# Performance work log

Hardware: AMD Instinct MI355X
Metric: run time of the kernel (lower is better)

Reference implementation:

```python
import jax, jax.numpy as jnp
import numpy as np

B, S, D, H = 8, 512, 1024, 8
DPH = D // H            # 128, dim per head
MAX_REL = 32
NGRAM = 2               # 2-gram RNN on heads 4..7
NG_START, NG_COUNT = 4, 4
SCALE = float(DPH) ** 0.5


def setup_inputs() -> dict:
    key = jax.random.key(0)
    ks = jax.random.split(key, 12)
    w = lambda k, shp: jax.random.normal(k, shp, jnp.float32) * 0.02
    return {
        "x": jax.random.normal(ks[0], (B, S, D), jnp.float32),
        "mask": jax.random.randint(ks[1], (B, 1, S), 0, 2).astype(bool),
        "Wq": w(ks[2], (D, D)), "bq": jnp.zeros((D,), jnp.float32),
        "Wk": w(ks[3], (D, D)), "bk": jnp.zeros((D,), jnp.float32),
        "Wv": w(ks[4], (D, D)), "bv": jnp.zeros((D,), jnp.float32),
        "Wo": w(ks[5], (D, D)), "bo": jnp.zeros((D,), jnp.float32),
        "rel_emb": w(ks[6], (2 * MAX_REL + 1, DPH)),
        "Wih_f": w(ks[7], (DPH, DPH)), "Whh_f": w(ks[8], (DPH, DPH)),
        "bih_f": jnp.zeros((DPH,), jnp.float32), "bhh_f": jnp.zeros((DPH,), jnp.float32),
        "Wih_b": w(ks[9], (DPH, DPH)), "Whh_b": w(ks[10], (DPH, DPH)),
        "bih_b": jnp.zeros((DPH,), jnp.float32), "bhh_b": jnp.zeros((DPH,), jnp.float32),
    }


def reference(x, mask, Wq, bq, Wk, bk, Wv, bv, Wo, bo, rel_emb,
              Wih_f, Whh_f, bih_f, bhh_f, Wih_b, Whh_b, bih_b, bhh_b):
    shape_h = lambda t: t.reshape(B, S, H, DPH).transpose(0, 2, 1, 3)  # [B,H,S,d]
    q = shape_h(x @ Wq.T + bq)
    k = shape_h(x @ Wk.T + bk)
    v = shape_h(x @ Wv.T + bv)

    # --- ngram path: zero masked positions in q/k/v (all heads) ---
    m = mask[:, :, :, None]  # [B,1,S,1] broadcast over heads and d
    q = jnp.where(m, 0.0, q)
    k = jnp.where(m, 0.0, k)
    v = jnp.where(m, 0.0, v)

    # per-head 2-gram bidirectional RNN on heads NG_START..NG_START+NG_COUNT-1
    qh = q[:, NG_START:NG_START + NG_COUNT].reshape(-1, S, DPH)
    kh = k[:, NG_START:NG_START + NG_COUNT].reshape(-1, S, DPH)
    vh = v[:, NG_START:NG_START + NG_COUNT].reshape(-1, S, DPH)
    feats = jnp.concatenate([qh, kh, vh], axis=0)          # [3*B*NG_COUNT, S, d]
    shifted = jnp.pad(feats, ((0, 0), (1, 0), (0, 0)))[:, :-1]  # shift-by-1 (prev token)
    seq = jnp.stack([shifted, feats], axis=0).reshape(NGRAM, -1, DPH)  # [T, N*S, d]
    h0 = jnp.zeros((seq.shape[1], DPH), jnp.float32)
    fstep = lambda h, xt: (jnp.tanh(xt @ Wih_f.T + bih_f + h @ Whh_f.T + bhh_f), None)
    bstep = lambda h, xt: (jnp.tanh(xt @ Wih_b.T + bih_b + h @ Whh_b.T + bhh_b), None)
    hf, _ = jax.lax.scan(fstep, h0, seq)            # fwd final hidden
    hb, _ = jax.lax.scan(bstep, h0, seq[::-1])      # bwd final hidden
    yy = (hf + hb).reshape(3, B, NG_COUNT, S, DPH)  # sum of direction finals
    q = q.at[:, NG_START:NG_START + NG_COUNT].set(yy[0])
    k = k.at[:, NG_START:NG_START + NG_COUNT].set(yy[1])
    v = v.at[:, NG_START:NG_START + NG_COUNT].set(yy[2])

    # --- relative-position attention ---
    qs = q / SCALE
    r = jnp.arange(S)
    rel_idx = jnp.clip(r[None, :] - r[:, None], -MAX_REL, MAX_REL) + MAX_REL  # [S,S]
    rel_k = rel_emb[rel_idx]  # [S,S,d]; same table used for keys and values
    scores = jnp.einsum('bhqd,bhkd->bhqk', qs, k) + jnp.einsum('bhqd,qkd->bhqk', qs, rel_k)
    scores = jnp.where(mask[:, None], -1e18, scores)  # [B,1,1,S] broadcast
    attn = jax.nn.softmax(scores, axis=-1)
    ctx = jnp.einsum('bhqk,bhkd->bhqd', attn, v) + jnp.einsum('bhqk,qkd->bhqd', attn, rel_k)
    out = ctx.transpose(0, 2, 1, 3).reshape(B, S, D) @ Wo.T + bo
    return out, attn
```

## Files before the change

### kernel.cpp

```cpp
#include <hip/hip_runtime.h>


typedef __bf16 bf16x8 __attribute__((ext_vector_type(8)));
typedef float f32x4 __attribute__((ext_vector_type(4)));

#define MFMA16(a, b, c) __builtin_amdgcn_mfma_f32_16x16x32_bf16(a, b, c, 0, 0, 0)

__device__ __forceinline__ unsigned short f2bf(float f) {
  unsigned u = __float_as_uint(f);
  u += 0x7FFFu + ((u >> 16) & 1u);
  return (unsigned short)(u >> 16);
}
__device__ __forceinline__ uint2 pack4(float4 f) {
  uint2 r;
  r.x = (unsigned)f2bf(f.x) | ((unsigned)f2bf(f.y) << 16);
  r.y = (unsigned)f2bf(f.z) | ((unsigned)f2bf(f.w) << 16);
  return r;
}
__device__ __forceinline__ void gld16(const unsigned short* g, unsigned short* l) {
  __builtin_amdgcn_global_load_lds(
      (const __attribute__((address_space(1))) unsigned int*)g,
      (__attribute__((address_space(3))) unsigned int*)l, 16, 0, 0);
}

__global__ __launch_bounds__(256) void prep_bf16(
    const float* __restrict__ x,
    const float* __restrict__ Wq, const float* __restrict__ Wk,
    const float* __restrict__ Wv,
    const float* __restrict__ Wihf, const float* __restrict__ Whhf,
    const float* __restrict__ Wihb, const float* __restrict__ Whhb,
    unsigned short* __restrict__ xb, unsigned short* __restrict__ Wqkvb,
    unsigned short* __restrict__ Wrnnb) {
  int i = blockIdx.x * 256 + threadIdx.x;
  const float* src;
  unsigned short* dst;
  int off;
  if (i < 1048576) {
    src = x; dst = xb; off = i;
  } else if (i < 1310720) {
    src = Wq; dst = Wqkvb; off = i - 1048576;
  } else if (i < 1572864) {
    src = Wk; dst = Wqkvb + 1048576; off = i - 1310720;
  } else if (i < 1835008) {
    src = Wv; dst = Wqkvb + 2097152; off = i - 1572864;
  } else if (i < 1839104) {
    src = Wihf; dst = Wrnnb; off = i - 1835008;
  } else if (i < 1843200) {
    src = Whhf; dst = Wrnnb + 16384; off = i - 1839104;
  } else if (i < 1847296) {
    src = Wihb; dst = Wrnnb + 32768; off = i - 1843200;
  } else {
    src = Whhb; dst = Wrnnb + 49152; off = i - 1847296;
  }
  float4 f = *((const float4*)src + off);
  *(uint2*)(dst + (size_t)off * 4) = pack4(f);
}

__global__ __launch_bounds__(256) void qkv_proj(
    const unsigned short* __restrict__ xb, const unsigned short* __restrict__ Wqkvb,
    const float* __restrict__ bq, const float* __restrict__ bk,
    const float* __restrict__ bv, const int* __restrict__ mask,
    unsigned short* __restrict__ qb, unsigned short* __restrict__ kb,
    unsigned short* __restrict__ vb, unsigned short* __restrict__ vT) {
  __shared__ __align__(16) unsigned short As[128 * 64];
  __shared__ __align__(16) unsigned short Bs[128 * 64];
  const int bm = blockIdx.x & 31;
  const int bn = blockIdx.x >> 5;
  const int t = bn >> 3;
  const int nloc0 = (bn & 7) * 128;
  const unsigned short* W = Wqkvb + (size_t)t * 1048576;
  const float* bias = (t == 0) ? bq : (t == 1) ? bk : bv;
  const int tid = threadIdx.x;
  const int lane = tid & 63, w = tid >> 6;
  const int wm = (w >> 1) * 64, wn = (w & 1) * 64;
  const int lanelo = lane & 15, quad = lane >> 4;
  const int row0 = bm * 128;
  const int rloc = lane >> 3, pch = lane & 7;
  const int lch = (pch - rloc) & 7;

  f32x4 acc[4][4];
  const f32x4 zf = {0.f, 0.f, 0.f, 0.f};
#pragma unroll
  for (int i = 0; i < 4; ++i)
#pragma unroll
    for (int j = 0; j < 4; ++j) acc[i][j] = zf;

  for (int kt = 0; kt < 16; ++kt) {
#pragma unroll
    for (int q = 0; q < 4; ++q) {
      int seg = w * 4 + q;
      int grow = seg * 8 + rloc;
      gld16(xb + (size_t)(row0 + grow) * 1024 + kt * 64 + lch * 8, &As[seg * 512]);
      gld16(W + (size_t)(nloc0 + grow) * 1024 + kt * 64 + lch * 8, &Bs[seg * 512]);
    }
    __syncthreads();
#pragma unroll
    for (int ks = 0; ks < 2; ++ks) {
      const int pA = (ks * 4 + quad + lanelo) & 7;
      bf16x8 a[4], bb[4];
#pragma unroll
      for (int i = 0; i < 4; ++i)
        a[i] = *(const bf16x8*)(&As[(wm + i * 16 + lanelo) * 64 + pA * 8]);
#pragma unroll
      for (int j = 0; j < 4; ++j)
        bb[j] = *(const bf16x8*)(&Bs[(wn + j * 16 + lanelo) * 64 + pA * 8]);
#pragma unroll
      for (int i = 0; i < 4; ++i)
#pragma unroll
        for (int j = 0; j < 4; ++j) acc[i][j] = MFMA16(a[i], bb[j], acc[i][j]);
    }
    __syncthreads();
  }
#pragma unroll
  for (int i = 0; i < 4; ++i) {
#pragma unroll
    for (int j = 0; j < 4; ++j) {
      int jj = nloc0 + wn + j * 16 + lanelo;
      int hh = jj >> 7, dc = jj & 127;
      float bvv = bias[jj];
      int m0 = row0 + wm + i * 16 + quad * 4;
      int b0 = m0 >> 9, sS = m0 & 511;
      unsigned short ov[4];
#pragma unroll
      for (int r = 0; r < 4; ++r) {
        int s = sS + r;
        float val = acc[i][j][r] + bvv;
        if (mask[b0 * 512 + s]) val = 0.f;
        unsigned short o = f2bf(val);
        ov[r] = o;
        size_t off = ((size_t)(b0 * 8 + hh) * 512 + s) * 128 + dc;
        if (t == 0) qb[off] = o;
        else if (t == 1) kb[off] = o;
        else vb[off] = o;
      }
      if (t == 2) {
        uint2 pk;
        pk.x = (unsigned)ov[0] | ((unsigned)ov[1] << 16);
        pk.y = (unsigned)ov[2] | ((unsigned)ov[3] << 16);
        *(uint2*)(&vT[((size_t)(b0 * 8 + hh) * 128 + dc) * 512 + sS]) = pk;
      }
    }
  }
}

__global__ __launch_bounds__(256) void prep_rel(
    const float* __restrict__ rel, unsigned short* __restrict__ relb,
    unsigned short* __restrict__ relT) {
  int i = blockIdx.x * 256 + threadIdx.x;
  if (i < 65 * 128) relb[i] = f2bf(rel[i]);
  if (i < 128 * 96) {
    int d = i / 96, r = i - d * 96;
    relT[i] = (r < 65) ? f2bf(rel[r * 128 + d]) : (unsigned short)0;
  }
}

__global__ __launch_bounds__(256) void rnn_fused(
    const unsigned short* __restrict__ qb, const unsigned short* __restrict__ kb,
    const unsigned short* __restrict__ vb,
    const unsigned short* __restrict__ Wrnnb,
    const float* __restrict__ bihf, const float* __restrict__ bhhf,
    const float* __restrict__ bihb, const float* __restrict__ bhhb,
    unsigned short* __restrict__ rnn_out) {
  __shared__ __align__(16) unsigned short X[65 * 136];
  __shared__ __align__(16) unsigned short Wi[128 * 136];
  __shared__ __align__(16) unsigned short Wh[128 * 136];
  __shared__ __align__(16) unsigned short H1[64 * 136];
  __shared__ float cbf[128], cbb[128];

  const unsigned short* Wihfb = Wrnnb;
  const unsigned short* Whhfb = Wrnnb + 16384;
  const unsigned short* Wihbb = Wrnnb + 32768;
  const unsigned short* Whhbb = Wrnnb + 49152;

  const int gid = blockIdx.x;
  const int tile = gid & 7;
  const int g = gid >> 3;
  const int t = g >> 5;
  const int rem = g & 31;
  const int b = rem >> 2, h = (rem & 3) + 4;
  const int s0 = tile * 64;
  const unsigned short* src = (t == 0) ? qb : (t == 1) ? kb : vb;
  const size_t rowbase = (size_t)(b * 8 + h) * 512;
  const int tid = threadIdx.x;

  for (int c = tid; c < 65 * 16; c += 256) {
    int r = c >> 4, cc = c & 15;
    uint4 v4;
    if (r == 0 && s0 == 0) v4 = make_uint4(0, 0, 0, 0);
    else v4 = *(const uint4*)(src + (rowbase + (s0 - 1 + r)) * 128 + cc * 8);
    *(uint4*)(&X[r * 136 + cc * 8]) = v4;
  }
#pragma unroll
  for (int p = 0; p < 8; ++p) {
    int c = p * 256 + tid;
    int r = c >> 4, cc = c & 15;
    *(uint4*)(&Wi[r * 136 + cc * 8]) = *(const uint4*)(Wihfb + c * 8);
    *(uint4*)(&Wh[r * 136 + cc * 8]) = *(const uint4*)(Whhfb + c * 8);
  }
  if (tid < 128) {
    cbf[tid] = bihf[tid] + bhhf[tid];
    cbb[tid] = bihb[tid] + bhhb[tid];
  }
  __syncthreads();

  const int lane = tid & 63, w = tid >> 6;
  const int lanelo = lane & 15, quad = lane >> 4;
  const int marow = w * 16 + lanelo;
  const f32x4 zf = {0.f, 0.f, 0.f, 0.f};

  f32x4 g1[8];
#pragma unroll
  for (int j = 0; j < 8; ++j) g1[j] = zf;
#pragma unroll
  for (int ks = 0; ks < 4; ++ks) {
    bf16x8 a = *(const bf16x8*)(&X[marow * 136 + ks * 32 + quad * 8]);
#pragma unroll
    for (int j = 0; j < 8; ++j) {
      bf16x8 bb = *(const bf16x8*)(&Wi[(j * 16 + lanelo) * 136 + ks * 32 + quad * 8]);
      g1[j] = MFMA16(a, bb, g1[j]);
    }
  }
#pragma unroll
  for (int j = 0; j < 8; ++j) {
    int col = j * 16 + lanelo;
    float cb = cbf[col];
#pragma unroll
    for (int i = 0; i < 4; ++i) {
      int row = w * 16 + quad * 4 + i;
      H1[row * 136 + col] = f2bf(tanhf(g1[j][i] + cb));
    }
  }
  __syncthreads();
  f32x4 a2[8];
#pragma unroll
  for (int j = 0; j < 8; ++j) a2[j] = zf;
#pragma unroll
  for (int ks = 0; ks < 4; ++ks) {
    bf16x8 a = *(const bf16x8*)(&X[(marow + 1) * 136 + ks * 32 + quad * 8]);
#pragma unroll
    for (int j = 0; j < 8; ++j) {
      bf16x8 bb = *(const bf16x8*)(&Wi[(j * 16 + lanelo) * 136 + ks * 32 + quad * 8]);
      a2[j] = MFMA16(a, bb, a2[j]);
    }
  }
#pragma unroll
  for (int ks = 0; ks < 4; ++ks) {
    bf16x8 a = *(const bf16x8*)(&H1[marow * 136 + ks * 32 + quad * 8]);
#pragma unroll
    for (int j = 0; j < 8; ++j) {
      bf16x8 bb = *(const bf16x8*)(&Wh[(j * 16 + lanelo) * 136 + ks * 32 + quad * 8]);
      a2[j] = MFMA16(a, bb, a2[j]);
    }
  }
  float outF[8][4];
#pragma unroll
  for (int j = 0; j < 8; ++j) {
    int col = j * 16 + lanelo;
    float cb = cbf[col];
#pragma unroll
    for (int i = 0; i < 4; ++i) outF[j][i] = tanhf(a2[j][i] + cb);
  }
  __syncthreads();
#pragma unroll
  for (int p = 0; p < 8; ++p) {
    int c = p * 256 + tid;
    int r = c >> 4, cc = c & 15;
    *(uint4*)(&Wi[r * 136 + cc * 8]) = *(const uint4*)(Wihbb + c * 8);
    *(uint4*)(&Wh[r * 136 + cc * 8]) = *(const uint4*)(Whhbb + c * 8);
  }
  __syncthreads();
#pragma unroll
  for (int j = 0; j < 8; ++j) g1[j] = zf;
#pragma unroll
  for (int ks = 0; ks < 4; ++ks) {
    bf16x8 a = *(const bf16x8*)(&X[(marow + 1) * 136 + ks * 32 + quad * 8]);
#pragma unroll
    for (int j = 0; j < 8; ++j) {
      bf16x8 bb = *(const bf16x8*)(&Wi[(j * 16 + lanelo) * 136 + ks * 32 + quad * 8]);
      g1[j] = MFMA16(a, bb, g1[j]);
    }
  }
#pragma unroll
  for (int j = 0; j < 8; ++j) {
    int col = j * 16 + lanelo;
    float cb = cbb[col];
#pragma unroll
    for (int i = 0; i < 4; ++i) {
      int row = w * 16 + quad * 4 + i;
      H1[row * 136 + col] = f2bf(tanhf(g1[j][i] + cb));
    }
  }
  __syncthreads();
#pragma unroll
  for (int j = 0; j < 8; ++j) a2[j] = zf;
#pragma unroll
  for (int ks = 0; ks < 4; ++ks) {
    bf16x8 a = *(const bf16x8*)(&X[marow * 136 + ks * 32 + quad * 8]);
#pragma unroll
    for (int j = 0; j < 8; ++j) {
      bf16x8 bb = *(const bf16x8*)(&Wi[(j * 16 + lanelo) * 136 + ks * 32 + quad * 8]);
      a2[j] = MFMA16(a, bb, a2[j]);
    }
  }
#pragma unroll
  for (int ks = 0; ks < 4; ++ks) {
    bf16x8 a = *(const bf16x8*)(&H1[marow * 136 + ks * 32 + quad * 8]);
#pragma unroll
    for (int j = 0; j < 8; ++j) {
      bf16x8 bb = *(const bf16x8*)(&Wh[(j * 16 + lanelo) * 136 + ks * 32 + quad * 8]);
      a2[j] = MFMA16(a, bb, a2[j]);
    }
  }
#pragma unroll
  for (int j = 0; j < 8; ++j) {
    int col = j * 16 + lanelo;
    float cb = cbb[col];
#pragma unroll
    for (int i = 0; i < 4; ++i) {
      int row = w * 16 + quad * 4 + i;
      float val = outF[j][i] + tanhf(a2[j][i] + cb);
      rnn_out[((size_t)g * 512 + s0 + row) * 128 + col] = f2bf(val);
    }
  }
}

__global__ __launch_bounds__(256) void rnn_copyback(
    const unsigned short* __restrict__ rnn_out,
    unsigned short* __restrict__ qb, unsigned short* __restrict__ kb,
    unsigned short* __restrict__ vT) {
  int idx = blockIdx.x * 256 + threadIdx.x;
  int g = idx >> 16;
  int r2 = idx & 65535;
  int s = r2 >> 7, col = r2 & 127;
  int t = g >> 5, rem = g & 31, b = rem >> 2, h = (rem & 3) + 4;
  unsigned short val = rnn_out[idx];
  size_t off = ((size_t)(b * 8 + h) * 512 + s) * 128 + col;
  if (t == 0) qb[off] = val;
  else if (t == 1) kb[off] = val;
  else vT[((size_t)(b * 8 + h) * 128 + col) * 512 + s] = val;
}

__global__ __launch_bounds__(256) void scores_av_fused(
    const unsigned short* __restrict__ qbuf, const unsigned short* __restrict__ kbuf,
    const unsigned short* __restrict__ relb, const unsigned short* __restrict__ vT,
    const unsigned short* __restrict__ relT, const float* __restrict__ relf,
    const int* __restrict__ mask, float* __restrict__ attn_out,
    unsigned short* __restrict__ ctx) {
  __shared__ __align__(16) char smem[40960];
  unsigned short* As = (unsigned short*)smem;
  float* Ps = (float*)(smem + 8704);
  float* cmaskS = (float*)(smem + 19456);
  unsigned short* attnb = (unsigned short*)smem;
  unsigned short* abufT = (unsigned short*)(smem + 32768);
  float* redb = (float*)(smem + 36864);

  const int idx = blockIdx.x;
  const int qt = idx >> 6, bh = idx & 63, b = bh >> 3;
  const int q0 = qt * 32;
  const size_t qrow0 = (size_t)bh * 512 + q0;
  const int tid = threadIdx.x;
  const int lane = tid & 63, w = tid >> 6;
  const int lanelo = lane & 15, quad = lane >> 4;
  const f32x4 zf = {0.f, 0.f, 0.f, 0.f};

  for (int c = tid; c < 512; c += 256) {
    int r = c >> 4, cc = c & 15;
    *(uint4*)(&As[r * 136 + cc * 8]) = *(const uint4*)(qbuf + (qrow0 + r) * 128 + cc * 8);
  }
  for (int i = tid; i < 512; i += 256) cmaskS[i] = mask[b * 512 + i] ? -1e9f : 0.f;
  if (tid < 256) *(uint4*)(&abufT[tid * 8]) = make_uint4(0, 0, 0, 0);
  __syncthreads();

  if (w < 2) {
    f32x4 pacc[5];
#pragma unroll
    for (int j = 0; j < 5; ++j) pacc[j] = zf;
#pragma unroll
    for (int ks = 0; ks < 4; ++ks) {
      bf16x8 qf_ = *(const bf16x8*)(&As[(w * 16 + lanelo) * 136 + ks * 32 + quad * 8]);
#pragma unroll
      for (int j = 0; j < 5; ++j) {
        int r = j * 16 + lanelo;
        uint4 tmp = make_uint4(0, 0, 0, 0);
        if (r < 65) tmp = *(const uint4*)(relb + r * 128 + ks * 32 + quad * 8);
        bf16x8 rf_ = *(bf16x8*)&tmp;
        pacc[j] = MFMA16(rf_, qf_, pacc[j]);
      }
    }
#pragma unroll
    for (int j = 0; j < 5; ++j)
      *(f32x4*)(&Ps[(w * 16 + lanelo) * 84 + j * 16 + quad * 4]) = pacc[j];
  }
  __syncthreads();

  f32x4 acc[8][2];
#pragma unroll
  for (int kf = 0; kf < 8; ++kf)
#pragma unroll
    for (int nf = 0; nf < 2; ++nf) acc[kf][nf] = zf;
  const unsigned short* kbp = kbuf + (size_t)bh * 65536;
#pragma unroll
  for (int ks = 0; ks < 4; ++ks) {
    bf16x8 qfr[2];
#pragma unroll
    for (int nf = 0; nf < 2; ++nf)
      qfr[nf] = *(const bf16x8*)(&As[(nf * 16 + lanelo) * 136 + ks * 32 + quad * 8]);
    bf16x8 kfr[8];
#pragma unroll
    for (int kf = 0; kf < 8; ++kf)
      kfr[kf] = *(const bf16x8*)(kbp + (size_t)((w * 8 + kf) * 16 + lanelo) * 128 +
                                 ks * 32 + quad * 8);
#pragma unroll
    for (int kf = 0; kf < 8; ++kf)
#pragma unroll
      for (int nf = 0; nf < 2; ++nf) acc[kf][nf] = MFMA16(kfr[kf], qfr[nf], acc[kf][nf]);
  }

  const float rscale = 0.08838834764831845f;
  float pmax[2] = {-3e38f, -3e38f};
#pragma unroll
  for (int qf = 0; qf < 2; ++qf) {
    const int q = qf * 16 + lanelo;
    const int qg = q0 + q;
    const float* PsR = &Ps[q * 84];
    const float p0 = PsR[0], p64 = PsR[64];
    const int qgmin = q0 + qf * 16;
#pragma unroll
    for (int kf = 0; kf < 8; ++kf) {
      const int kmin = w * 128 + kf * 16;
      const int kbase = kmin + quad * 4;
      if (kmin + 15 - qgmin <= -32) {
#pragma unroll
        for (int i = 0; i < 4; ++i) {
          float val = (acc[kf][qf][i] + p0) * rscale + cmaskS[kbase + i];
          acc[kf][qf][i] = val;
          pmax[qf] = fmaxf(pmax[qf], val);
        }
      } else if (kmin - (qgmin + 15) >= 32) {
#pragma unroll
        for (int i = 0; i < 4; ++i) {
          float val = (acc[kf][qf][i] + p64) * rscale + cmaskS[kbase + i];
          acc[kf][qf][i] = val;
          pmax[qf] = fmaxf(pmax[qf], val);
        }
      } else {
#pragma unroll
        for (int i = 0; i < 4; ++i) {
          int k = kbase + i;
          int d = k - qg;
          int r = min(max(d, -32), 32) + 32;
          float val = (acc[kf][qf][i] + PsR[r]) * rscale + cmaskS[k];
          acc[kf][qf][i] = val;
          pmax[qf] = fmaxf(pmax[qf], val);
        }
      }
    }
  }
  float* red_max = redb;
  float* red_sum = redb + 256;
  float* red_s0 = redb + 512;
  float* red_s64 = redb + 768;
#pragma unroll
  for (int qf = 0; qf < 2; ++qf) {
    pmax[qf] = fmaxf(pmax[qf], __shfl_xor(pmax[qf], 16, 64));
    pmax[qf] = fmaxf(pmax[qf], __shfl_xor(pmax[qf], 32, 64));
  }
  if (quad == 0) {
#pragma unroll
    for (int qf = 0; qf < 2; ++qf) red_max[w * 64 + qf * 16 + lanelo] = pmax[qf];
  }
  __syncthreads();
  float mf_[2], psum[2];
#pragma unroll
  for (int qf = 0; qf < 2; ++qf) {
    int q = qf * 16 + lanelo;
    mf_[qf] = fmaxf(fmaxf(red_max[q], red_max[64 + q]),
                    fmaxf(red_max[128 + q], red_max[192 + q]));
    psum[qf] = 0.f;
  }
#pragma unroll
  for (int qf = 0; qf < 2; ++qf)
#pragma unroll
    for (int kf = 0; kf < 8; ++kf)
#pragma unroll
      for (int i = 0; i < 4; ++i) {
        float e = __expf(acc[kf][qf][i] - mf_[qf]);
        acc[kf][qf][i] = e;
        psum[qf] += e;
      }
#pragma unroll
  for (int qf = 0; qf < 2; ++qf) {
    psum[qf] += __shfl_xor(psum[qf], 16, 64);
    psum[qf] += __shfl_xor(psum[qf], 32, 64);
  }
  if (quad == 0) {
#pragma unroll
    for (int qf = 0; qf < 2; ++qf) red_sum[w * 64 + qf * 16 + lanelo] = psum[qf];
  }
  __syncthreads();
  float rs[2];
#pragma unroll
  for (int qf = 0; qf < 2; ++qf) {
    int q = qf * 16 + lanelo;
    float s = red_sum[q] + red_sum[64 + q] + red_sum[128 + q] + red_sum[192 + q];
    rs[qf] = (s > 0.f) ? 1.f / s : 0.f;
  }

  float s0p[2] = {0.f, 0.f}, s64p[2] = {0.f, 0.f};
#pragma unroll
  for (int qf = 0; qf < 2; ++qf) {
    const int q = qf * 16 + lanelo;
    const int qg = q0 + q;
    const int qgmin = q0 + qf * 16;
#pragma unroll
    for (int kf = 0; kf < 8; ++kf) {
      const int kmin = w * 128 + kf * 16;
      const int kbase = kmin + quad * 4;
      float4 at;
      float* ap = (float*)&at;
#pragma unroll
      for (int i = 0; i < 4; ++i) ap[i] = acc[kf][qf][i] * rs[qf];
      if (kmin + 15 - qgmin <= -32) {
#pragma unroll
        for (int i = 0; i < 4; ++i) s0p[qf] += ap[i];
      } else if (kmin - (qgmin + 15) >= 32) {
#pragma unroll
        for (int i = 0; i < 4; ++i) s64p[qf] += ap[i];
      } else {
#pragma unroll
        for (int i = 0; i < 4; ++i) {
          int d = kbase + i - qg;
          if (d <= -32) s0p[qf] += ap[i];
          else if (d >= 32) s64p[qf] += ap[i];
          else {
            int col = d + 32;
            abufT[q * 64 + (((col >> 3) + q) & 7) * 8 + (col & 7)] = f2bf(ap[i]);
          }
        }
      }
      *(float4*)(&attn_out[((size_t)bh * 512 + qg) * 512 + kbase]) = at;
      uint2 pk = pack4(at);
      int cc = kbase >> 3;
      *(uint2*)(&attnb[q * 512 + ((cc + q) & 63) * 8 + (quad & 1) * 4]) = pk;
    }
  }
#pragma unroll
  for (int qf = 0; qf < 2; ++qf) {
    s0p[qf] += __shfl_xor(s0p[qf], 16, 64);
    s0p[qf] += __shfl_xor(s0p[qf], 32, 64);
    s64p[qf] += __shfl_xor(s64p[qf], 16, 64);
    s64p[qf] += __shfl_xor(s64p[qf], 32, 64);
  }
  if (quad == 0) {
#pragma unroll
    for (int qf = 0; qf < 2; ++qf) {
      red_s0[w * 64 + qf * 16 + lanelo] = s0p[qf];
      red_s64[w * 64 + qf * 16 + lanelo] = s64p[qf];
    }
  }
  __syncthreads();
  float s0f[2], s64f[2];
#pragma unroll
  for (int qf = 0; qf < 2; ++qf) {
    int q = qf * 16 + lanelo;
    s0f[qf] = red_s0[q] + red_s0[64 + q] + red_s0[128 + q] + red_s0[192 + q];
    s64f[qf] = red_s64[q] + red_s64[64 + q] + red_s64[128 + q] + red_s64[192 + q];
  }

  f32x4 cacc[2][2];
#pragma unroll
  for (int mf = 0; mf < 2; ++mf)
#pragma unroll
    for (int nf = 0; nf < 2; ++nf) cacc[mf][nf] = zf;
  const unsigned short* vbp = vT + (size_t)bh * 65536;
#pragma unroll
  for (int kt = 0; kt < 16; ++kt) {
    bf16x8 afr[2], bfr[2];
#pragma unroll
    for (int mf = 0; mf < 2; ++mf)
      afr[mf] = *(const bf16x8*)(vbp + (size_t)((w * 2 + mf) * 16 + lanelo) * 512 +
                                 kt * 32 + quad * 8);
#pragma unroll
    for (int nf = 0; nf < 2; ++nf) {
      int q = nf * 16 + lanelo;
      bfr[nf] = *(const bf16x8*)(&attnb[q * 512 + ((kt * 4 + quad + q) & 63) * 8]);
    }
#pragma unroll
    for (int mf = 0; mf < 2; ++mf)
#pragma unroll
      for (int nf = 0; nf < 2; ++nf) cacc[mf][nf] = MFMA16(afr[mf], bfr[nf], cacc[mf][nf]);
  }
#pragma unroll
  for (int kt = 16; kt < 18; ++kt) {
    bf16x8 afr[2], bfr[2];
#pragma unroll
    for (int mf = 0; mf < 2; ++mf)
      afr[mf] = *(const bf16x8*)(relT + ((w * 2 + mf) * 16 + lanelo) * 96 +
                                 (kt - 16) * 32 + quad * 8);
#pragma unroll
    for (int nf = 0; nf < 2; ++nf) {
      int q = nf * 16 + lanelo;
      bfr[nf] = *(const bf16x8*)(&abufT[q * 64 + (((kt - 16) * 4 + quad + q) & 7) * 8]);
    }
#pragma unroll
    for (int mf = 0; mf < 2; ++mf)
#pragma unroll
      for (int nf = 0; nf < 2; ++nf) cacc[mf][nf] = MFMA16(afr[mf], bfr[nf], cacc[mf][nf]);
  }

  float r0v[2][4], r64v[2][4];
#pragma unroll
  for (int mf = 0; mf < 2; ++mf)
#pragma unroll
    for (int i = 0; i < 4; ++i) {
      int d = w * 32 + mf * 16 + quad * 4 + i;
      r0v[mf][i] = relf[d];
      r64v[mf][i] = relf[64 * 128 + d];
    }
  const int b_ = bh >> 3, h_ = bh & 7;
#pragma unroll
  for (int nf = 0; nf < 2; ++nf) {
    int qg = q0 + nf * 16 + lanelo;
#pragma unroll
    for (int mf = 0; mf < 2; ++mf) {
      unsigned short ov[4];
#pragma unroll
      for (int i = 0; i < 4; ++i) {
        float val = cacc[mf][nf][i] + s0f[nf] * r0v[mf][i] + s64f[nf] * r64v[mf][i];
        ov[i] = f2bf(val);
      }
      uint2 pk;
      pk.x = (unsigned)ov[0] | ((unsigned)ov[1] << 16);
      pk.y = (unsigned)ov[2] | ((unsigned)ov[3] << 16);
      *(uint2*)(&ctx[((size_t)(b_ * 512 + qg)) * 1024 + h_ * 128 + w * 32 + mf * 16 + quad * 4]) = pk;
    }
  }
}

__global__ __launch_bounds__(256) void out_proj(
    const unsigned short* __restrict__ ctx, const float* __restrict__ Wo,
    const float* __restrict__ bo, float* __restrict__ outp) {
  __shared__ __align__(16) unsigned short As[128 * 64];
  __shared__ __align__(16) unsigned short Bs[128 * 64];
  const int bm = blockIdx.x & 31, bn = blockIdx.x >> 5;
  const int tid = threadIdx.x, lane = tid & 63, w = tid >> 6;
  const int wm = (w >> 1) * 64, wn = (w & 1) * 64;
  const int lanelo = lane & 15, quad = lane >> 4;
  const int row0 = bm * 128, col0 = bn * 128;
  const int rloc = lane >> 3, pch = lane & 7;
  const int lch = (pch - rloc) & 7;
  f32x4 acc[4][4];
  const f32x4 zf = {0.f, 0.f, 0.f, 0.f};
#pragma unroll
  for (int i = 0; i < 4; ++i)
#pragma unroll
    for (int j = 0; j < 4; ++j) acc[i][j] = zf;

  for (int kt = 0; kt < 16; ++kt) {
#pragma unroll
    for (int q = 0; q < 4; ++q) {
      int seg = w * 4 + q;
      int grow = seg * 8 + rloc;
      gld16(ctx + (size_t)(row0 + grow) * 1024 + kt * 64 + lch * 8, &As[seg * 512]);
    }
    for (int c = tid; c < 1024; c += 256) {
      int r = c >> 3, cc2 = c & 7;
      const float* src = Wo + (size_t)(col0 + r) * 1024 + kt * 64 + cc2 * 8;
      int pc = (cc2 + r) & 7;
      *(uint2*)(&Bs[r * 64 + pc * 8]) = pack4(*(const float4*)src);
      *(uint2*)(&Bs[r * 64 + pc * 8 + 4]) = pack4(*(const float4*)(src + 4));
    }
    __syncthreads();
#pragma unroll
    for (int ks = 0; ks < 2; ++ks) {
      const int pA = (ks * 4 + quad + lanelo) & 7;
      bf16x8 a[4], bb[4];
#pragma unroll
      for (int i = 0; i < 4; ++i)
        a[i] = *(const bf16x8*)(&As[(wm + i * 16 + lanelo) * 64 + pA * 8]);
#pragma unroll
      for (int j = 0; j < 4; ++j)
        bb[j] = *(const bf16x8*)(&Bs[(wn + j * 16 + lanelo) * 64 + pA * 8]);
#pragma unroll
      for (int i = 0; i < 4; ++i)
#pragma unroll
        for (int j = 0; j < 4; ++j) acc[i][j] = MFMA16(a[i], bb[j], acc[i][j]);
    }
    __syncthreads();
  }
#pragma unroll
  for (int i = 0; i < 4; ++i) {
#pragma unroll
    for (int j = 0; j < 4; ++j) {
      int n = col0 + wn + j * 16 + lanelo;
      float bbv = bo[n];
#pragma unroll
      for (int r = 0; r < 4; ++r) {
        int m = row0 + wm + i * 16 + quad * 4 + r;
        outp[(size_t)m * 1024 + n] = acc[i][j][r] + bbv;
      }
    }
  }
}

extern "C" void kernel_launch(void* const* d_in, const int* in_sizes, int n_in,
                              void* d_out, int out_size, void* d_ws, size_t ws_size,
                              hipStream_t stream) {
  const float* x    = (const float*)d_in[0];
  const int*   mask = (const int*)d_in[1];
  const float* Wq   = (const float*)d_in[2];
  const float* bq   = (const float*)d_in[3];
  const float* Wk   = (const float*)d_in[4];
  const float* bk   = (const float*)d_in[5];
  const float* Wv   = (const float*)d_in[6];
  const float* bv   = (const float*)d_in[7];
  const float* Wo   = (const float*)d_in[8];
  const float* bo   = (const float*)d_in[9];
  const float* rel  = (const float*)d_in[10];
  const float* Wihf = (const float*)d_in[11];
  const float* Whhf = (const float*)d_in[12];
  const float* bihf = (const float*)d_in[13];
  const float* bhhf = (const float*)d_in[14];
  const float* Wihb = (const float*)d_in[15];
  const float* Whhb = (const float*)d_in[16];
  const float* bihb = (const float*)d_in[17];
  const float* bhhb = (const float*)d_in[18];

  char* ws = (char*)d_ws;
  unsigned short* qb   = (unsigned short*)(ws + 0);
  unsigned short* kb   = (unsigned short*)(ws + 8388608);
  unsigned short* vT   = (unsigned short*)(ws + 16777216);
  unsigned short* ctx  = (unsigned short*)(ws + 25165824);
  unsigned short* relb = (unsigned short*)(ws + 33554432);
  unsigned short* relT = (unsigned short*)(ws + 33571072);

  float* outp  = (float*)d_out;
  float* attnF = outp + 4194304;
  unsigned short* abase  = (unsigned short*)attnF;
  unsigned short* xb     = abase;
  unsigned short* vb     = abase + 4194304;
  unsigned short* rnnout = abase + 8388608;
  unsigned short* Wqkvb  = abase + 14680064;
  unsigned short* Wrnnb  = abase + 17825792;

  prep_bf16<<<dim3(7232), dim3(256), 0, stream>>>(
      x, Wq, Wk, Wv, Wihf, Whhf, Wihb, Whhb, xb, Wqkvb, Wrnnb);
  prep_rel<<<dim3(48), dim3(256), 0, stream>>>(rel, relb, relT);
  qkv_proj<<<dim3(768), dim3(256), 0, stream>>>(xb, Wqkvb, bq, bk, bv, mask,
                                                qb, kb, vb, vT);
  rnn_fused<<<dim3(768), dim3(256), 0, stream>>>(qb, kb, vb, Wrnnb,
                                                 bihf, bhhf, bihb, bhhb, rnnout);
  rnn_copyback<<<dim3(24576), dim3(256), 0, stream>>>(rnnout, qb, kb, vT);
  scores_av_fused<<<dim3(1024), dim3(256), 0, stream>>>(qb, kb, relb, vT, relT,
                                                        rel, mask, attnF, ctx);
  out_proj<<<dim3(256), dim3(256), 0, stream>>>(ctx, Wo, bo, outp);
}
```

Measured before the change: 359.0 us.

## Fuse RNN copyback into rnn_fused via tile boundary buffer and read weights from global

The separate rnn_copyback kernel and its intermediate rnn_out buffer are removed. rnn_fused now writes its results in place into q/k and transposed V. To avoid a read-after-write race on the previous-token row at tile edges, qkv_proj saves each tile's last row into a small boundary buffer that aliases ctx. The RNN weight matrices are no longer staged in LDS and are read straight from global/L2, and the two input-weight GEMMs are merged into one pass, which drops several __syncthreads. This saves a launch and a full round trip through memory, at the cost of uncached global weight loads inside the MFMA loops.

```diff
diff --git a/kernel.cpp b/kernel.cpp
--- a/kernel.cpp
+++ b/kernel.cpp
@@ -61,7 +61,8 @@
     const float* __restrict__ bq, const float* __restrict__ bk,
     const float* __restrict__ bv, const int* __restrict__ mask,
     unsigned short* __restrict__ qb, unsigned short* __restrict__ kb,
-    unsigned short* __restrict__ vb, unsigned short* __restrict__ vT) {
+    unsigned short* __restrict__ vb, unsigned short* __restrict__ vT,
+    unsigned short* __restrict__ bnd) {
   __shared__ __align__(16) unsigned short As[128 * 64];
   __shared__ __align__(16) unsigned short Bs[128 * 64];
   const int bm = blockIdx.x & 31;
@@ -132,6 +133,8 @@
         if (t == 0) qb[off] = o;
         else if (t == 1) kb[off] = o;
         else vb[off] = o;
+        if (((s & 63) == 63) && s != 511 && hh >= 4)
+          bnd[((size_t)(t * 32 + b0 * 4 + (hh - 4)) * 7 + (s >> 6)) * 128 + dc] = o;
       }
       if (t == 2) {
         uint2 pk;
@@ -155,15 +158,13 @@
 }
 
 __global__ __launch_bounds__(256) void rnn_fused(
-    const unsigned short* __restrict__ qb, const unsigned short* __restrict__ kb,
+    unsigned short* __restrict__ qb, unsigned short* __restrict__ kb,
     const unsigned short* __restrict__ vb,
     const unsigned short* __restrict__ Wrnnb,
     const float* __restrict__ bihf, const float* __restrict__ bhhf,
     const float* __restrict__ bihb, const float* __restrict__ bhhb,
-    unsigned short* __restrict__ rnn_out) {
+    const unsigned short* __restrict__ bnd, unsigned short* __restrict__ vT) {
   __shared__ __align__(16) unsigned short X[65 * 136];
-  __shared__ __align__(16) unsigned short Wi[128 * 136];
-  __shared__ __align__(16) unsigned short Wh[128 * 136];
   __shared__ __align__(16) unsigned short H1[64 * 136];
   __shared__ float cbf[128], cbb[128];
 
@@ -186,16 +187,13 @@
   for (int c = tid; c < 65 * 16; c += 256) {
     int r = c >> 4, cc = c & 15;
     uint4 v4;
-    if (r == 0 && s0 == 0) v4 = make_uint4(0, 0, 0, 0);
-    else v4 = *(const uint4*)(src + (rowbase + (s0 - 1 + r)) * 128 + cc * 8);
+    if (r == 0) {
+      if (s0 == 0) v4 = make_uint4(0, 0, 0, 0);
+      else v4 = *(const uint4*)(bnd + ((size_t)g * 7 + (tile - 1)) * 128 + cc * 8);
+    } else {
+      v4 = *(const uint4*)(src + (rowbase + (s0 - 1 + r)) * 128 + cc * 8);
+    }
     *(uint4*)(&X[r * 136 + cc * 8]) = v4;
-  }
-#pragma unroll
-  for (int p = 0; p < 8; ++p) {
-    int c = p * 256 + tid;
-    int r = c >> 4, cc = c & 15;
-    *(uint4*)(&Wi[r * 136 + cc * 8]) = *(const uint4*)(Wihfb + c * 8);
-    *(uint4*)(&Wh[r * 136 + cc * 8]) = *(const uint4*)(Whhfb + c * 8);
   }
   if (tid < 128) {
     cbf[tid] = bihf[tid] + bhhf[tid];
@@ -206,18 +204,22 @@
   const int lane = tid & 63, w = tid >> 6;
   const int lanelo = lane & 15, quad = lane >> 4;
   const int marow = w * 16 + lanelo;
+  const int wfoff = lanelo * 128 + quad * 8;
   const f32x4 zf = {0.f, 0.f, 0.f, 0.f};
 
-  f32x4 g1[8];
-#pragma unroll
-  for (int j = 0; j < 8; ++j) g1[j] = zf;
+  f32x4 g1[8], a2[8];
+#pragma unroll
+  for (int j = 0; j < 8; ++j) { g1[j] = zf; a2[j] = zf; }
+
 #pragma unroll
   for (int ks = 0; ks < 4; ++ks) {
-    bf16x8 a = *(const bf16x8*)(&X[marow * 136 + ks * 32 + quad * 8]);
+    bf16x8 ap = *(const bf16x8*)(&X[marow * 136 + ks * 32 + quad * 8]);
+    bf16x8 ac = *(const bf16x8*)(&X[(marow + 1) * 136 + ks * 32 + quad * 8]);
 #pragma unroll
     for (int j = 0; j < 8; ++j) {
-      bf16x8 bb = *(const bf16x8*)(&Wi[(j * 16 + lanelo) * 136 + ks * 32 + quad * 8]);
-      g1[j] = MFMA16(a, bb, g1[j]);
+      bf16x8 bb = *(const bf16x8*)(Wihfb + j * 2048 + ks * 32 + wfoff);
+      g1[j] = MFMA16(ap, bb, g1[j]);
+      a2[j] = MFMA16(ac, bb, a2[j]);
     }
   }
 #pragma unroll
@@ -230,25 +232,12 @@
       H1[row * 136 + col] = f2bf(tanhf(g1[j][i] + cb));
     }
   }
-  __syncthreads();
-  f32x4 a2[8];
-#pragma unroll
-  for (int j = 0; j < 8; ++j) a2[j] = zf;
-#pragma unroll
-  for (int ks = 0; ks < 4; ++ks) {
-    bf16x8 a = *(const bf16x8*)(&X[(marow + 1) * 136 + ks * 32 + quad * 8]);
-#pragma unroll
-    for (int j = 0; j < 8; ++j) {
-      bf16x8 bb = *(const bf16x8*)(&Wi[(j * 16 + lanelo) * 136 + ks * 32 + quad * 8]);
-      a2[j] = MFMA16(a, bb, a2[j]);
-    }
-  }
 #pragma unroll
   for (int ks = 0; ks < 4; ++ks) {
     bf16x8 a = *(const bf16x8*)(&H1[marow * 136 + ks * 32 + quad * 8]);
 #pragma unroll
     for (int j = 0; j < 8; ++j) {
-      bf16x8 bb = *(const bf16x8*)(&Wh[(j * 16 + lanelo) * 136 + ks * 32 + quad * 8]);
+      bf16x8 bb = *(const bf16x8*)(Whhfb + j * 2048 + ks * 32 + wfoff);
       a2[j] = MFMA16(a, bb, a2[j]);
     }
   }
@@ -260,24 +249,17 @@
 #pragma unroll
     for (int i = 0; i < 4; ++i) outF[j][i] = tanhf(a2[j][i] + cb);
   }
-  __syncthreads();
-#pragma unroll
-  for (int p = 0; p < 8; ++p) {
-    int c = p * 256 + tid;
-    int r = c >> 4, cc = c & 15;
-    *(uint4*)(&Wi[r * 136 + cc * 8]) = *(const uint4*)(Wihbb + c * 8);
-    *(uint4*)(&Wh[r * 136 + cc * 8]) = *(const uint4*)(Whhbb + c * 8);
-  }
-  __syncthreads();
-#pragma unroll
-  for (int j = 0; j < 8; ++j) g1[j] = zf;
+#pragma unroll
+  for (int j = 0; j < 8; ++j) { g1[j] = zf; a2[j] = zf; }
 #pragma unroll
   for (int ks = 0; ks < 4; ++ks) {
-    bf16x8 a = *(const bf16x8*)(&X[(marow + 1) * 136 + ks * 32 + quad * 8]);
+    bf16x8 ap = *(const bf16x8*)(&X[marow * 136 + ks * 32 + quad * 8]);
+    bf16x8 ac = *(const bf16x8*)(&X[(marow + 1) * 136 + ks * 32 + quad * 8]);
 #pragma unroll
     for (int j = 0; j < 8; ++j) {
-      bf16x8 bb = *(const bf16x8*)(&Wi[(j * 16 + lanelo) * 136 + ks * 32 + quad * 8]);
-      g1[j] = MFMA16(a, bb, g1[j]);
+      bf16x8 bb = *(const bf16x8*)(Wihbb + j * 2048 + ks * 32 + wfoff);
+      g1[j] = MFMA16(ac, bb, g1[j]);
+      a2[j] = MFMA16(ap, bb, a2[j]);
     }
   }
 #pragma unroll
@@ -290,24 +272,12 @@
       H1[row * 136 + col] = f2bf(tanhf(g1[j][i] + cb));
     }
   }
-  __syncthreads();
-#pragma unroll
-  for (int j = 0; j < 8; ++j) a2[j] = zf;
-#pragma unroll
-  for (int ks = 0; ks < 4; ++ks) {
-    bf16x8 a = *(const bf16x8*)(&X[marow * 136 + ks * 32 + quad * 8]);
-#pragma unroll
-    for (int j = 0; j < 8; ++j) {
-      bf16x8 bb = *(const bf16x8*)(&Wi[(j * 16 + lanelo) * 136 + ks * 32 + quad * 8]);
-      a2[j] = MFMA16(a, bb, a2[j]);
-    }
-  }
 #pragma unroll
   for (int ks = 0; ks < 4; ++ks) {
     bf16x8 a = *(const bf16x8*)(&H1[marow * 136 + ks * 32 + quad * 8]);
 #pragma unroll
     for (int j = 0; j < 8; ++j) {
-      bf16x8 bb = *(const bf16x8*)(&Wh[(j * 16 + lanelo) * 136 + ks * 32 + quad * 8]);
+      bf16x8 bb = *(const bf16x8*)(Whhbb + j * 2048 + ks * 32 + wfoff);
       a2[j] = MFMA16(a, bb, a2[j]);
     }
   }
@@ -315,29 +285,25 @@
   for (int j = 0; j < 8; ++j) {
     int col = j * 16 + lanelo;
     float cb = cbb[col];
+    unsigned short ov[4];
 #pragma unroll
     for (int i = 0; i < 4; ++i) {
-      int row = w * 16 + quad * 4 + i;
       float val = outF[j][i] + tanhf(a2[j][i] + cb);
-      rnn_out[((size_t)g * 512 + s0 + row) * 128 + col] = f2bf(val);
-    }
-  }
-}
-
-__global__ __launch_bounds__(256) void rnn_copyback(
-    const unsigned short* __restrict__ rnn_out,
-    unsigned short* __restrict__ qb, unsigned short* __restrict__ kb,
-    unsigned short* __restrict__ vT) {
-  int idx = blockIdx.x * 256 + threadIdx.x;
-  int g = idx >> 16;
-  int r2 = idx & 65535;
-  int s = r2 >> 7, col = r2 & 127;
-  int t = g >> 5, rem = g & 31, b = rem >> 2, h = (rem & 3) + 4;
-  unsigned short val = rnn_out[idx];
-  size_t off = ((size_t)(b * 8 + h) * 512 + s) * 128 + col;
-  if (t == 0) qb[off] = val;
-  else if (t == 1) kb[off] = val;
-  else vT[((size_t)(b * 8 + h) * 128 + col) * 512 + s] = val;
+      ov[i] = f2bf(val);
+    }
+    int row0l = w * 16 + quad * 4;
+    if (t == 2) {
+      uint2 pk;
+      pk.x = (unsigned)ov[0] | ((unsigned)ov[1] << 16);
+      pk.y = (unsigned)ov[2] | ((unsigned)ov[3] << 16);
+      *(uint2*)(&vT[((size_t)(b * 8 + h) * 128 + col) * 512 + s0 + row0l]) = pk;
+    } else {
+      unsigned short* dst = (t == 0) ? qb : kb;
+#pragma unroll
+      for (int i = 0; i < 4; ++i)
+        dst[(rowbase + s0 + row0l + i) * 128 + col] = ov[i];
+    }
+  }
 }
 
 __global__ __launch_bounds__(256) void scores_av_fused(
@@ -733,13 +699,13 @@
   unsigned short* ctx  = (unsigned short*)(ws + 25165824);
   unsigned short* relb = (unsigned short*)(ws + 33554432);
   unsigned short* relT = (unsigned short*)(ws + 33571072);
+  unsigned short* bnd  = ctx;
 
   float* outp  = (float*)d_out;
   float* attnF = outp + 4194304;
   unsigned short* abase  = (unsigned short*)attnF;
   unsigned short* xb     = abase;
   unsigned short* vb     = abase + 4194304;
-  unsigned short* rnnout = abase + 8388608;
   unsigned short* Wqkvb  = abase + 14680064;
   unsigned short* Wrnnb  = abase + 17825792;
 
@@ -747,10 +713,9 @@
       x, Wq, Wk, Wv, Wihf, Whhf, Wihb, Whhb, xb, Wqkvb, Wrnnb);
   prep_rel<<<dim3(48), dim3(256), 0, stream>>>(rel, relb, relT);
   qkv_proj<<<dim3(768), dim3(256), 0, stream>>>(xb, Wqkvb, bq, bk, bv, mask,
-                                                qb, kb, vb, vT);
+                                                qb, kb, vb, vT, bnd);
   rnn_fused<<<dim3(768), dim3(256), 0, stream>>>(qb, kb, vb, Wrnnb,
-                                                 bihf, bhhf, bihb, bhhb, rnnout);
-  rnn_copyback<<<dim3(24576), dim3(256), 0, stream>>>(rnnout, qb, kb, vT);
+                                                 bihf, bhhf, bihb, bhhb, bnd, vT);
   scores_av_fused<<<dim3(1024), dim3(256), 0, stream>>>(qb, kb, relb, vT, relT,
                                                         rel, mask, attnF, ctx);
   out_proj<<<dim3(256), dim3(256), 0, stream>>>(ctx, Wo, bo, outp);
```

Result: slower. 452.2 us (+25.9%).
